# Kernel tuning notes

Measured on AMD Instinct MI355X. Metric: run time of the kernel, lower is better.

## Reference

```python
import jax, jax.numpy as jnp
import numpy as np

N, M = 1048576, 64  # rows (vector length), columns to orthogonalize (dim=-1)


def setup_inputs() -> dict:
    key = jax.random.key(0)
    X = jax.random.normal(key, (N, M), dtype=jnp.float32)
    return {"X": X}


def _gram_schmidt(X):
    # Modified Gram-Schmidt along the last dim, matching the torch module:
    # torch.select returns a view, so `v -= ...` updates v in place between
    # successive projections -> modified (sequential) Gram-Schmidt.
    n, m = X.shape
    result = jnp.zeros_like(X)
    result = result.at[:, 0].set(X[:, 0] / jnp.linalg.norm(X[:, 0]))
    for i in range(1, m):  # static loop over small fixed column count
        v = X[:, i]

        def body(j, v, result=result):
            r_j = jax.lax.dynamic_slice(result, (0, j), (n, 1))[:, 0]
            return v - jnp.dot(v, r_j) * r_j  # sequential MGS update

        v = jax.lax.fori_loop(0, i, body, v)
        result = result.at[:, i].set(v / jnp.linalg.norm(v))
    return result


def reference(X):
    return _gram_schmidt(X)
```

## Files before the change

kernel.cpp:

```cpp
#include <hip/hip_runtime.h>
#include <hip/hip_bf16.h>

#define MDIM 64

typedef __attribute__((ext_vector_type(8))) short short8;
typedef __attribute__((ext_vector_type(4))) float f32x4;

__device__ __forceinline__ unsigned short bf16_of(float x) {
  __hip_bfloat16 b = __float2bfloat16(x);
  return *reinterpret_cast<unsigned short*>(&b);
}
__device__ __forceinline__ float f32_of(unsigned short h) {
  return __uint_as_float(((unsigned int)h) << 16);
}
__device__ __forceinline__ void split2(float x, short& h, short& l) {
  unsigned short hh = bf16_of(x);
  h = (short)hh;
  l = (short)bf16_of(x - f32_of(hh));
}

__global__ __launch_bounds__(256) void k_gram(const float* __restrict__ X,
                                              float* __restrict__ partials,
                                              int N, int cpw) {
  __shared__ float red[2][4096];
  const int t = threadIdx.x;
  const int lane = t & 63;
  const int wave = t >> 6;
  const int gw = blockIdx.x * 4 + wave;
  const int col = lane & 15;
  const int kg = lane >> 4;

  f32x4 acc[16];
#pragma unroll
  for (int i = 0; i < 16; ++i) acc[i] = (f32x4){0.f, 0.f, 0.f, 0.f};

  for (int c = 0; c < cpw; ++c) {
    long r0 = ((long)gw * cpw + c) * 32;
    if (r0 >= N) break;
    short8 fh[4], fl[4];
#pragma unroll
    for (int b = 0; b < 4; ++b) {
      const float* p = X + (r0 + kg * 8) * MDIM + b * 16 + col;
#pragma unroll
      for (int e = 0; e < 8; ++e) {
        long r = r0 + kg * 8 + e;
        float x = (r < N) ? p[e * MDIM] : 0.f;
        short h, l;
        split2(x, h, l);
        fh[b][e] = h;
        fl[b][e] = l;
      }
    }
#pragma unroll
    for (int bi = 0; bi < 4; ++bi)
#pragma unroll
      for (int bj = 0; bj < 4; ++bj) {
        int idx = bi * 4 + bj;
        acc[idx] = __builtin_amdgcn_mfma_f32_16x16x32_bf16(fh[bi], fh[bj], acc[idx], 0, 0, 0);
        acc[idx] = __builtin_amdgcn_mfma_f32_16x16x32_bf16(fh[bi], fl[bj], acc[idx], 0, 0, 0);
        acc[idx] = __builtin_amdgcn_mfma_f32_16x16x32_bf16(fl[bi], fh[bj], acc[idx], 0, 0, 0);
      }
  }

  if (wave < 2) {
#pragma unroll
    for (int bi = 0; bi < 4; ++bi)
#pragma unroll
      for (int bj = 0; bj < 4; ++bj)
#pragma unroll
        for (int q = 0; q < 4; ++q)
          red[wave][(bi * 16 + kg * 4 + q) * MDIM + bj * 16 + col] = acc[bi * 4 + bj][q];
  }
  __syncthreads();
  if (wave >= 2) {
    float* dst = red[wave - 2];
#pragma unroll
    for (int bi = 0; bi < 4; ++bi)
#pragma unroll
      for (int bj = 0; bj < 4; ++bj)
#pragma unroll
        for (int q = 0; q < 4; ++q)
          dst[(bi * 16 + kg * 4 + q) * MDIM + bj * 16 + col] += acc[bi * 4 + bj][q];
  }
  __syncthreads();
  float* p = partials + (long)blockIdx.x * 4096;
  for (int e = t; e < 4096; e += 256) p[e] = red[0][e] + red[1][e];
}

__global__ __launch_bounds__(256) void k_reduce1(const float* __restrict__ partials,
                                                 float* __restrict__ P2, int nblk) {
  int g = blockIdx.x * 256 + threadIdx.x;
  int e = g & 4095, s = g >> 12;
  int p0 = (nblk * s) >> 4, p1 = (nblk * (s + 1)) >> 4;
  float sum = 0.f;
  for (int p = p0; p < p1; ++p) sum += partials[(long)p * 4096 + e];
  P2[g] = sum;
}

__global__ __launch_bounds__(256) void k_reduce2(const float* __restrict__ P2,
                                                 float* __restrict__ G) {
  int e = blockIdx.x * 256 + threadIdx.x;
  float sum = 0.f;
#pragma unroll
  for (int s = 0; s < 16; ++s) sum += P2[s * 4096 + e];
  G[e] = sum;
}

__global__ __launch_bounds__(64) void k_cholinv(const float* __restrict__ G,
                                                unsigned short* __restrict__ Rh,
                                                unsigned short* __restrict__ Rl) {
  __shared__ float Ls[64][65];
  __shared__ float colbuf[64];
  __shared__ float invd[64];
  const int t = threadIdx.x;

  {
    float row[64];
#pragma unroll
    for (int j4 = 0; j4 < 16; ++j4)
      *reinterpret_cast<f32x4*>(&row[j4 * 4]) =
          *reinterpret_cast<const f32x4*>(G + t * MDIM + j4 * 4);

#pragma unroll
    for (int k = 0; k < 64; ++k) {
      colbuf[t] = row[k];
      __syncthreads();
      float inv = 1.f / sqrtf(colbuf[k]);
      if (t == 0) invd[k] = inv;
      float lk = row[k] * inv;
      row[k] = lk;
      Ls[t][k] = lk;
#pragma unroll
      for (int j = k + 1; j < 64; ++j)
        row[j] = fmaf(-lk, colbuf[j] * inv, row[j]);
      __syncthreads();
    }
  }

  float y[64];
#pragma unroll
  for (int i = 0; i < 64; ++i) {
    float s = 0.f;
#pragma unroll
    for (int m = 0; m < i; ++m) s = fmaf(Ls[i][m], y[m], s);
    y[i] = (i == t) ? invd[i] : -invd[i] * s;
  }

#pragma unroll
  for (int j = 0; j < 64; ++j) {
    float v = y[j];
    unsigned short h = bf16_of(v);
    Rh[t * MDIM + j] = h;
    Rl[t * MDIM + j] = bf16_of(v - f32_of(h));
  }
}

__global__ __launch_bounds__(256) void k_apply(const float* __restrict__ X,
                                               const unsigned short* __restrict__ Rh,
                                               const unsigned short* __restrict__ Rl,
                                               float* __restrict__ Q, int N) {
  const int t = threadIdx.x;
  const int lane = t & 63;
  const int wave = t >> 6;
  const int col = lane & 15;
  const int kg = lane >> 4;

  short8 bh[4][2], bl[4][2];
#pragma unroll
  for (int jb = 0; jb < 4; ++jb)
#pragma unroll
    for (int kc = 0; kc < 2; ++kc)
#pragma unroll
      for (int e = 0; e < 8; ++e) {
        int k = kc * 32 + kg * 8 + e;
        bh[jb][kc][e] = (short)Rh[k * MDIM + jb * 16 + col];
        bl[jb][kc][e] = (short)Rl[k * MDIM + jb * 16 + col];
      }

  long base = ((long)blockIdx.x * 4 + wave) * 256;
#pragma unroll 1
  for (int i = 0; i < 16; ++i) {
    long r0 = base + i * 16;
    if (r0 >= N) break;
    long rr = r0 + col;
    if (rr > N - 1) rr = N - 1;
    const float* xp = X + rr * MDIM + kg * 8;

    short8 ah[2], al[2];
#pragma unroll
    for (int kc = 0; kc < 2; ++kc) {
      float xv[8];
      *reinterpret_cast<f32x4*>(&xv[0]) = *reinterpret_cast<const f32x4*>(xp + kc * 32);
      *reinterpret_cast<f32x4*>(&xv[4]) = *reinterpret_cast<const f32x4*>(xp + kc * 32 + 4);
#pragma unroll
      for (int e = 0; e < 8; ++e) {
        short h, l;
        split2(xv[e], h, l);
        ah[kc][e] = h;
        al[kc][e] = l;
      }
    }

    f32x4 q[4];
#pragma unroll
    for (int jb = 0; jb < 4; ++jb) q[jb] = (f32x4){0.f, 0.f, 0.f, 0.f};
#pragma unroll
    for (int jb = 0; jb < 4; ++jb)
#pragma unroll
      for (int kc = 0; kc < 2; ++kc) {
        q[jb] = __builtin_amdgcn_mfma_f32_16x16x32_bf16(ah[kc], bh[jb][kc], q[jb], 0, 0, 0);
        q[jb] = __builtin_amdgcn_mfma_f32_16x16x32_bf16(ah[kc], bl[jb][kc], q[jb], 0, 0, 0);
        q[jb] = __builtin_amdgcn_mfma_f32_16x16x32_bf16(al[kc], bh[jb][kc], q[jb], 0, 0, 0);
      }

#pragma unroll
    for (int jb = 0; jb < 4; ++jb)
#pragma unroll
      for (int qq = 0; qq < 4; ++qq) {
        long orow = r0 + kg * 4 + qq;
        if (orow < N) Q[orow * MDIM + jb * 16 + col] = q[jb][qq];
      }
  }
}

extern "C" void kernel_launch(void* const* d_in, const int* in_sizes, int n_in,
                              void* d_out, int out_size, void* d_ws, size_t ws_size,
                              hipStream_t stream) {
  const float* X = (const float*)d_in[0];
  float* Q = (float*)d_out;
  const int N = in_sizes[0] / MDIM;

  float* ws = (float*)d_ws;
  float* G = ws;
  float* P2 = ws + 4096;
  unsigned short* Rh = (unsigned short*)(ws + 69632);
  unsigned short* Rl = (unsigned short*)(ws + 71680);
  float* partials = ws + 73728;

  const int nwave = 4096;
  int chunks = (N + 31) / 32;
  int cpw = (chunks + nwave - 1) / nwave;

  k_gram<<<1024, 256, 0, stream>>>(X, partials, N, cpw);
  k_reduce1<<<256, 256, 0, stream>>>(partials, P2, 1024);
  k_reduce2<<<16, 256, 0, stream>>>(P2, G);
  k_cholinv<<<1, 64, 0, stream>>>(G, Rh, Rl);
  k_apply<<<(int)((N + 1023) / 1024), 256, 0, stream>>>(X, Rh, Rl, Q, N);
}
```

Baseline: 597.1 us.

## Restructure Gram kernel: coalesced loads via LDS transpose, symmetric tiles, per-wave blocks

The Gram-matrix kernel now runs one wave per block. Each wave loads 32-row chunks of X as coalesced float4 reads and transposes them through padded shared memory to build the MFMA fragments, replacing the old strided scalar column loads. Only the upper-triangular 10 of 16 tiles are computed, and the reduction kernel remaps indices to rebuild the symmetric matrix. The in-block cross-wave LDS reduction is gone and a template removes bounds checks when N divides evenly, at the cost of more partial blocks to reduce and extra syncs per chunk.

```diff
diff --git a/kernel.cpp b/kernel.cpp
--- a/kernel.cpp
+++ b/kernel.cpp
@@ -19,81 +19,88 @@
   l = (short)bf16_of(x - f32_of(hh));
 }
 
-__global__ __launch_bounds__(256) void k_gram(const float* __restrict__ X,
-                                              float* __restrict__ partials,
-                                              int N, int cpw) {
-  __shared__ float red[2][4096];
-  const int t = threadIdx.x;
-  const int lane = t & 63;
-  const int wave = t >> 6;
-  const int gw = blockIdx.x * 4 + wave;
-  const int col = lane & 15;
-  const int kg = lane >> 4;
-
-  f32x4 acc[16];
-#pragma unroll
-  for (int i = 0; i < 16; ++i) acc[i] = (f32x4){0.f, 0.f, 0.f, 0.f};
+template<bool GUARD>
+__global__ __launch_bounds__(64, 4) void k_gram(const float* __restrict__ X,
+                                                float* __restrict__ partials,
+                                                long N, int cpw) {
+  __shared__ float xsT[64 * 33];
+  const int l = threadIdx.x;
+  const int col = l & 15;
+  const int kg = l >> 4;
+
+  f32x4 acc[10];
+#pragma unroll
+  for (int i = 0; i < 10; ++i) acc[i] = (f32x4){0.f, 0.f, 0.f, 0.f};
+
+  const long wrow0 = (long)blockIdx.x * cpw * 32;
 
   for (int c = 0; c < cpw; ++c) {
-    long r0 = ((long)gw * cpw + c) * 32;
-    if (r0 >= N) break;
+    long r0 = wrow0 + (long)c * 32;
+    if (GUARD && r0 >= N) break;
+
+    f32x4 st[8];
+#pragma unroll
+    for (int i = 0; i < 8; ++i) {
+      long r = r0 + i * 4 + kg;
+      if (!GUARD || r < N)
+        st[i] = *reinterpret_cast<const f32x4*>(X + r * MDIM + col * 4);
+      else
+        st[i] = (f32x4){0.f, 0.f, 0.f, 0.f};
+    }
+#pragma unroll
+    for (int i = 0; i < 8; ++i) {
+      int r = i * 4 + kg;
+#pragma unroll
+      for (int j = 0; j < 4; ++j)
+        xsT[(col * 4 + j) * 33 + r] = st[i][j];
+    }
+    __syncthreads();
+
     short8 fh[4], fl[4];
 #pragma unroll
     for (int b = 0; b < 4; ++b) {
-      const float* p = X + (r0 + kg * 8) * MDIM + b * 16 + col;
+      const float* src = &xsT[(b * 16 + col) * 33 + kg * 8];
 #pragma unroll
       for (int e = 0; e < 8; ++e) {
-        long r = r0 + kg * 8 + e;
-        float x = (r < N) ? p[e * MDIM] : 0.f;
-        short h, l;
-        split2(x, h, l);
+        short h, lo;
+        split2(src[e], h, lo);
         fh[b][e] = h;
-        fl[b][e] = l;
-      }
-    }
-#pragma unroll
-    for (int bi = 0; bi < 4; ++bi)
-#pragma unroll
-      for (int bj = 0; bj < 4; ++bj) {
-        int idx = bi * 4 + bj;
-        acc[idx] = __builtin_amdgcn_mfma_f32_16x16x32_bf16(fh[bi], fh[bj], acc[idx], 0, 0, 0);
-        acc[idx] = __builtin_amdgcn_mfma_f32_16x16x32_bf16(fh[bi], fl[bj], acc[idx], 0, 0, 0);
-        acc[idx] = __builtin_amdgcn_mfma_f32_16x16x32_bf16(fl[bi], fh[bj], acc[idx], 0, 0, 0);
-      }
-  }
-
-  if (wave < 2) {
-#pragma unroll
-    for (int bi = 0; bi < 4; ++bi)
-#pragma unroll
-      for (int bj = 0; bj < 4; ++bj)
-#pragma unroll
-        for (int q = 0; q < 4; ++q)
-          red[wave][(bi * 16 + kg * 4 + q) * MDIM + bj * 16 + col] = acc[bi * 4 + bj][q];
-  }
-  __syncthreads();
-  if (wave >= 2) {
-    float* dst = red[wave - 2];
-#pragma unroll
-    for (int bi = 0; bi < 4; ++bi)
-#pragma unroll
-      for (int bj = 0; bj < 4; ++bj)
-#pragma unroll
-        for (int q = 0; q < 4; ++q)
-          dst[(bi * 16 + kg * 4 + q) * MDIM + bj * 16 + col] += acc[bi * 4 + bj][q];
-  }
-  __syncthreads();
-  float* p = partials + (long)blockIdx.x * 4096;
-  for (int e = t; e < 4096; e += 256) p[e] = red[0][e] + red[1][e];
+        fl[b][e] = lo;
+      }
+    }
+    __syncthreads();
+
+#pragma unroll
+    for (int ti = 0; ti < 4; ++ti)
+#pragma unroll
+      for (int tj = ti; tj < 4; ++tj) {
+        const int idx = ti * 4 + tj - ((ti * (ti + 1)) >> 1);
+        acc[idx] = __builtin_amdgcn_mfma_f32_16x16x32_bf16(fh[ti], fh[tj], acc[idx], 0, 0, 0);
+        acc[idx] = __builtin_amdgcn_mfma_f32_16x16x32_bf16(fh[ti], fl[tj], acc[idx], 0, 0, 0);
+        acc[idx] = __builtin_amdgcn_mfma_f32_16x16x32_bf16(fl[ti], fh[tj], acc[idx], 0, 0, 0);
+      }
+  }
+
+  float* p = partials + (long)blockIdx.x * 2560;
+#pragma unroll
+  for (int tidx = 0; tidx < 10; ++tidx)
+#pragma unroll
+    for (int q = 0; q < 4; ++q)
+      p[tidx * 256 + (kg * 4 + q) * 16 + col] = acc[tidx][q];
 }
 
 __global__ __launch_bounds__(256) void k_reduce1(const float* __restrict__ partials,
                                                  float* __restrict__ P2, int nblk) {
   int g = blockIdx.x * 256 + threadIdx.x;
   int e = g & 4095, s = g >> 12;
+  int r = e >> 6, c = e & 63;
+  int bi = r >> 4, bj = c >> 4, ri = r & 15, ci = c & 15;
+  int off;
+  if (bi <= bj) off = (bi * 4 + bj - ((bi * (bi + 1)) >> 1)) * 256 + ri * 16 + ci;
+  else          off = (bj * 4 + bi - ((bj * (bj + 1)) >> 1)) * 256 + ci * 16 + ri;
   int p0 = (nblk * s) >> 4, p1 = (nblk * (s + 1)) >> 4;
   float sum = 0.f;
-  for (int p = p0; p < p1; ++p) sum += partials[(long)p * 4096 + e];
+  for (int p = p0; p < p1; ++p) sum += partials[(long)p * 2560 + off];
   P2[g] = sum;
 }
 
@@ -158,7 +165,7 @@
 __global__ __launch_bounds__(256) void k_apply(const float* __restrict__ X,
                                                const unsigned short* __restrict__ Rh,
                                                const unsigned short* __restrict__ Rl,
-                                               float* __restrict__ Q, int N) {
+                                               float* __restrict__ Q, long N) {
   const int t = threadIdx.x;
   const int lane = t & 63;
   const int wave = t >> 6;
@@ -228,7 +235,7 @@
                               hipStream_t stream) {
   const float* X = (const float*)d_in[0];
   float* Q = (float*)d_out;
-  const int N = in_sizes[0] / MDIM;
+  const long N = in_sizes[0] / MDIM;
 
   float* ws = (float*)d_ws;
   float* G = ws;
@@ -237,12 +244,14 @@
   unsigned short* Rl = (unsigned short*)(ws + 71680);
   float* partials = ws + 73728;
 
-  const int nwave = 4096;
-  int chunks = (N + 31) / 32;
-  int cpw = (chunks + nwave - 1) / nwave;
-
-  k_gram<<<1024, 256, 0, stream>>>(X, partials, N, cpw);
-  k_reduce1<<<256, 256, 0, stream>>>(partials, P2, 1024);
+  const long NBLK = 4096;
+  const long per = NBLK * 32;
+  bool exact = (N % per == 0);
+  int cpw = (int)((N + per - 1) / per);
+
+  if (exact) k_gram<false><<<NBLK, 64, 0, stream>>>(X, partials, N, cpw);
+  else       k_gram<true ><<<NBLK, 64, 0, stream>>>(X, partials, N, cpw);
+  k_reduce1<<<256, 256, 0, stream>>>(partials, P2, (int)NBLK);
   k_reduce2<<<16, 256, 0, stream>>>(P2, G);
   k_cholinv<<<1, 64, 0, stream>>>(G, Rh, Rl);
   k_apply<<<(int)((N + 1023) / 1024), 256, 0, stream>>>(X, Rh, Rl, Q, N);
```

Result: slower. 828.5 us (+38.8%).
